# Kernel tuning notes

Hardware: AMD Instinct MI355X
Metric: run time of the kernel (lower is better)

Reference implementation:

```python
import jax, jax.numpy as jnp
import numpy as np

N_NODES = 100000
N_EDGES = 1600000
N_GRAPHS = 5000
F_IN = 11
HID = 128
N_CLASSES = 19


def setup_inputs() -> dict:
    key = jax.random.key(0)
    ks = jax.random.split(key, 12)
    x = jax.random.normal(ks[0], (N_NODES, F_IN), dtype=jnp.float32)
    edge_index = jax.random.randint(ks[1], (2, N_EDGES), 0, N_NODES, dtype=jnp.int64)
    batch = jnp.sort(jax.random.randint(ks[2], (N_NODES,), 0, N_GRAPHS, dtype=jnp.int64))
    def glorot(k, shape):
        lim = float(np.sqrt(6.0 / (shape[0] + shape[1])))
        return jax.random.uniform(k, shape, jnp.float32, -lim, lim)
    return {
        'x': x,
        'edge_index': edge_index,
        'batch': batch,
        'W1': glorot(ks[3], (F_IN, HID)),  'b1': jnp.zeros((HID,), jnp.float32),
        'W2': glorot(ks[4], (HID, HID)),   'b2': jnp.zeros((HID,), jnp.float32),
        'W3': glorot(ks[5], (HID, HID)),   'b3': jnp.zeros((HID,), jnp.float32),
        'Wlin': glorot(ks[6], (HID, N_CLASSES)), 'blin': jnp.zeros((N_CLASSES,), jnp.float32),
    }


def _gcn_conv(x, src, dst, norm, self_w, W, b):
    # GCNConv: D^{-1/2}(A+I)D^{-1/2} X W + b  (self loops handled analytically)
    h = x @ W                                   # [N, out]
    msg = h[src] * norm[:, None]                # [E, out] gathered + scaled
    agg = jax.ops.segment_sum(msg, dst, num_segments=N_NODES)
    return agg + h * self_w[:, None] + b


def reference(x, edge_index, batch, W1, b1, W2, b2, W3, b3, Wlin, blin):
    src, dst = edge_index[0], edge_index[1]
    # degree including self loop (gcn_norm with add_self_loops=True)
    deg = jax.ops.segment_sum(jnp.ones((N_EDGES,), x.dtype), dst, num_segments=N_NODES) + 1.0
    dis = jax.lax.rsqrt(deg)                    # deg^{-1/2}
    norm = dis[src] * dis[dst]                  # per-edge coefficient
    self_w = dis * dis                          # 1/deg for the self loop

    h = jax.nn.relu(_gcn_conv(x, src, dst, norm, self_w, W1, b1))
    h = jax.nn.relu(_gcn_conv(h, src, dst, norm, self_w, W2, b2))
    h = _gcn_conv(h, src, dst, norm, self_w, W3, b3)

    # global_mean_pool over graph ids
    sums = jax.ops.segment_sum(h, batch, num_segments=N_GRAPHS)
    cnts = jax.ops.segment_sum(jnp.ones((N_NODES,), h.dtype), batch, num_segments=N_GRAPHS)
    pooled = sums / jnp.maximum(cnts, 1.0)[:, None]

    # dropout is identity in eval mode
    return pooled @ Wlin + blin
```

## Files before the change

kernel.cpp:

```cpp
#include <hip/hip_runtime.h>
#include <hip/hip_bf16.h>
#include <hip/hip_fp16.h>

#define NN 100000
#define NE 1600000
#define NG 5000
#define FIN 11
#define HID 128
#define NC 19

#define NBK 98
#define BKSH 10
#define BKMASK 1023
#define BCAP 20480
#define CCAP 24576

typedef _Float16 f16x8 __attribute__((ext_vector_type(8)));
typedef float f32x4 __attribute__((ext_vector_type(4)));


__global__ __launch_bounds__(1024) void k_p1scatter(const int* __restrict__ ei,
                                                    int* __restrict__ gcur, unsigned int* __restrict__ p1) {
    __shared__ int hist[NBK];
    __shared__ int base[NBK];
    __shared__ int lrank[NBK];
    int t = threadIdx.x;
    if (t < NBK) { hist[t] = 0; lrank[t] = 0; }
    __syncthreads();

    int e0 = blockIdx.x * 4096 + t * 4;
    int sr[4], dr[4], bk[4];
    if (e0 + 3 < NE) {
        int4 s4 = *(const int4*)(ei + e0);
        int4 d4 = *(const int4*)(ei + NE + e0);
        sr[0] = s4.x; sr[1] = s4.y; sr[2] = s4.z; sr[3] = s4.w;
        dr[0] = d4.x; dr[1] = d4.y; dr[2] = d4.z; dr[3] = d4.w;
        #pragma unroll
        for (int k = 0; k < 4; ++k) { bk[k] = dr[k] >> BKSH; atomicAdd(&hist[bk[k]], 1); }
    } else {
        #pragma unroll
        for (int k = 0; k < 4; ++k) {
            int e = e0 + k;
            if (e < NE) { sr[k] = ei[e]; dr[k] = ei[NE + e]; bk[k] = dr[k] >> BKSH; atomicAdd(&hist[bk[k]], 1); }
            else bk[k] = -1;
        }
    }
    __syncthreads();
    if (t < NBK && hist[t] > 0)
        base[t] = t * BCAP + atomicAdd(&gcur[t], hist[t]);
    __syncthreads();
    #pragma unroll
    for (int k = 0; k < 4; ++k) {
        if (bk[k] >= 0) {
            int slot = atomicAdd(&lrank[bk[k]], 1);
            p1[base[bk[k]] + slot] = (unsigned int)sr[k] | ((unsigned int)(dr[k] & BKMASK) << 17);
        }
    }
}

__global__ __launch_bounds__(1024) void k_p2fill(const unsigned int* __restrict__ p1,
                                                 const int* __restrict__ gcur,
                                                 unsigned int* __restrict__ meta, int* __restrict__ csr,
                                                 float* __restrict__ dis) {
    __shared__ int cnt[1024];
    __shared__ int pf[1024];
    __shared__ int cur[1024];
    __shared__ int wsum[16];
    int bkt = blockIdx.x;
    int t = threadIdx.x;
    int v0 = bkt << BKSH;
    int nb = NN - v0; if (nb > 1024) nb = 1024;
    cnt[t] = 0; cur[t] = 0;
    __syncthreads();
    int count = gcur[bkt]; if (count > BCAP) count = BCAP;
    const unsigned int* reg = p1 + (size_t)bkt * BCAP;
    for (int i = t; i < count; i += 1024)
        atomicAdd(&cnt[reg[i] >> 17], 1);
    __syncthreads();
    int c = cnt[t];
    int pc = (c + 3) & ~3;
    int lane = t & 63, w = t >> 6;
    int val = pc;
    #pragma unroll
    for (int off = 1; off < 64; off <<= 1) {
        int n = __shfl_up(val, off, 64);
        if (lane >= off) val += n;
    }
    if (lane == 63) wsum[w] = val;
    __syncthreads();
    if (w == 0) {
        int s = (lane < 16) ? wsum[lane] : 0;
        #pragma unroll
        for (int off = 1; off < 16; off <<= 1) {
            int n = __shfl_up(s, off, 64);
            if (lane >= off) s += n;
        }
        if (lane < 16) wsum[lane] = s;
    }
    __syncthreads();
    int wbase = (w == 0) ? 0 : wsum[w - 1];
    int excl = wbase + val - pc;
    pf[t] = excl;
    unsigned int gb = (unsigned int)bkt * CCAP;
    if (t < nb) {
        meta[v0 + t] = ((gb + (unsigned int)excl) << 9) | (unsigned int)(pc >> 2);
        dis[v0 + t] = rsqrtf((float)c + 1.0f);
    }
    __syncthreads();
    for (int i = t; i < count; i += 1024) {
        unsigned int u = reg[i];
        int dl = u >> 17;
        int off2 = atomicAdd(&cur[dl], 1);
        csr[gb + pf[dl] + off2] = (int)(u & 0x1FFFFu);
    }
    if (t < nb) {
        int b0 = gb + pf[t];
        for (int k = c; k < pc; ++k) csr[b0 + k] = NN;
    }
}


__global__ __launch_bounds__(256) void k_setup(const float* __restrict__ x, const float* __restrict__ dis,
                                               const int* __restrict__ batch,
                                               const float* __restrict__ W2, const float* __restrict__ W3,
                                               const float* __restrict__ b3, const float* __restrict__ Wl,
                                               const float* __restrict__ bl,
                                               _Float16* __restrict__ xsc, int* __restrict__ gstart,
                                               _Float16* __restrict__ Wp2, float* __restrict__ Wf,
                                               float* __restrict__ bf,
                                               _Float16* __restrict__ Ht, _Float16* __restrict__ tb16) {
    int b = blockIdx.x, t = threadIdx.x;
    if (b < 6251) {
        int i = b * 256 + t;
        if (i < (NN + 1) * 16) {
            int v = i >> 4, c = i & 15;
            float val = (v < NN && c < FIN) ? x[v * FIN + c] * dis[v] : 0.f;
            xsc[i] = (_Float16)val;
        }
    } else if (b < 6271) {
        int g = (b - 6251) * 256 + t;
        if (g > NG) return;
        int lo = 0, hi = NN;
        while (lo < hi) {
            int mid = (lo + hi) >> 1;
            if (batch[mid] < g) lo = mid + 1; else hi = mid;
        }
        gstart[g] = lo;
    } else if (b < 6279) {
        int t2 = (b - 6271) * 256 + t;
        int lane = t2 & 63;
        int tile = t2 >> 6;
        int kb = tile >> 3, ct = tile & 7;
        int kbase = kb * 32 + (lane >> 4) * 8;
        int col = ct * 16 + (lane & 15);
        f16x8 v;
        #pragma unroll
        for (int e = 0; e < 8; ++e) v[e] = (_Float16)W2[(kbase + e) * HID + col];
        *(f16x8*)&Wp2[(size_t)t2 * 8] = v;
    } else if (b < 6312) {
        int i = (b - 6279) * 4 + (t >> 6);
        int tc = t & 63;
        if (tc >= NC || i > HID) return;
        if (i < HID) {
            float a = 0.f;
            #pragma unroll 4
            for (int k = 0; k < HID; ++k) a += W3[i * HID + k] * Wl[k * NC + tc];
            Wf[i * NC + tc] = a;
        } else {
            float a = bl[tc];
            #pragma unroll 4
            for (int k = 0; k < HID; ++k) a += b3[k] * Wl[k * NC + tc];
            bf[tc] = a;
        }
    } else {
        if (t < HID) Ht[(size_t)NN * HID + t] = (_Float16)0.f;
        else tb16[(size_t)NN * HID + (t - HID)] = (_Float16)0.f;
    }
}

__global__ __launch_bounds__(256) void k_l1(const _Float16* __restrict__ xsc,
                                            const unsigned int* __restrict__ meta,
                                            const int* __restrict__ csr, const float* __restrict__ dis,
                                            const float* __restrict__ W1, const float* __restrict__ b1,
                                            _Float16* __restrict__ out16) {
    __shared__ float Ws[FIN][HID];
    __shared__ float Xs[16][17];
    int t = threadIdx.x;
    int row0 = blockIdx.x * 16;
    for (int idx = t; idx < FIN * HID; idx += 256) Ws[idx / HID][idx % HID] = W1[idx];

    int wave = t >> 6, lane = t & 63;
    int erel = lane >> 4, c = lane & 15;
    #pragma unroll
    for (int i = 0; i < 4; ++i) {
        int v = row0 + wave * 4 + i;
        unsigned int m = meta[v];
        int beg = (int)(m >> 9);
        int pend = beg + (int)((m & 511u) << 2);
        float accA = 0.f, accB = 0.f;
        int e = beg;
        for (; e + 8 <= pend; e += 8) {
            int s0 = csr[e + erel], s1 = csr[e + 4 + erel];
            accA += (float)xsc[s0 * 16 + c];
            accB += (float)xsc[s1 * 16 + c];
        }
        if (e < pend) accA += (float)xsc[csr[e + erel] * 16 + c];
        float a = accA + accB;
        a += __shfl_xor(a, 16);
        a += __shfl_xor(a, 32);
        if (erel == 0) {
            a += (float)xsc[v * 16 + c];
            Xs[wave * 4 + i][c] = a * dis[v];
        }
    }
    __syncthreads();
    int cc = t & (HID - 1);
    int rg = t >> 7;
    #pragma unroll
    for (int i = 0; i < 8; ++i) {
        int r = rg * 8 + i;
        int row = row0 + r;
        float a = b1[cc];
        #pragma unroll
        for (int k = 0; k < FIN; ++k) a += Xs[r][k] * Ws[k][cc];
        a = fmaxf(a, 0.f);
        out16[(size_t)row * HID + cc] = (_Float16)(a * dis[row]);
    }
}

__global__ __launch_bounds__(256) void k_agg16(const _Float16* __restrict__ Ht,
                                               const unsigned int* __restrict__ meta,
                                               const int* __restrict__ csr, const float* __restrict__ dis,
                                               _Float16* __restrict__ out16) {
    int wid = threadIdx.x >> 6;
    int lane = threadIdx.x & 63;
    int v = blockIdx.x * 4 + wid;
    if (v >= NN) return;
    int erel = lane >> 4;
    int c8 = lane & 15;
    const _Float16* bp = Ht + (size_t)c8 * 8;
    unsigned int m = meta[v];
    int beg = (int)(m >> 9);
    int pend = beg + (int)((m & 511u) << 2);
    float acc0[8] = {}, acc1[8] = {};
    int e = beg;
    for (; e + 16 <= pend; e += 16) {
        int s0 = csr[e + erel];
        int s1 = csr[e + 4 + erel];
        int s2 = csr[e + 8 + erel];
        int s3 = csr[e + 12 + erel];
        f16x8 h0 = *(const f16x8*)(bp + (size_t)s0 * HID);
        f16x8 h1 = *(const f16x8*)(bp + (size_t)s1 * HID);
        f16x8 h2 = *(const f16x8*)(bp + (size_t)s2 * HID);
        f16x8 h3 = *(const f16x8*)(bp + (size_t)s3 * HID);
        #pragma unroll
        for (int j = 0; j < 8; ++j) {
            acc0[j] += (float)h0[j] + (float)h2[j];
            acc1[j] += (float)h1[j] + (float)h3[j];
        }
    }
    for (; e < pend; e += 4) {
        int s = csr[e + erel];
        f16x8 h = *(const f16x8*)(bp + (size_t)s * HID);
        #pragma unroll
        for (int j = 0; j < 8; ++j) acc0[j] += (float)h[j];
    }
    #pragma unroll
    for (int j = 0; j < 8; ++j) {
        float s = acc0[j] + acc1[j];
        s += __shfl_xor(s, 16);
        s += __shfl_xor(s, 32);
        acc0[j] = s;
    }
    if (erel == 0) {
        f16x8 sh = *(const f16x8*)(bp + (size_t)v * HID);
        float dv = dis[v];
        f16x8 o;
        #pragma unroll
        for (int j = 0; j < 8; ++j) o[j] = (_Float16)((acc0[j] + (float)sh[j]) * dv);
        *(f16x8*)(out16 + (size_t)v * HID + c8 * 8) = o;
    }
}

__global__ __launch_bounds__(256) void k_gemm128m(const _Float16* __restrict__ X,
                                                  const _Float16* __restrict__ Wp,
                                                  const float* __restrict__ bias,
                                                  const float* __restrict__ dis,
                                                  _Float16* __restrict__ out) {
    int wave = threadIdx.x >> 6, lane = threadIdx.x & 63;
    int row0 = blockIdx.x * 128 + wave * 32;
    int rA = lane & 15, kg = lane >> 4;

    f32x4 acc[2][8];
    #pragma unroll
    for (int s = 0; s < 2; ++s)
        #pragma unroll
        for (int c = 0; c < 8; ++c)
            acc[s][c] = {0.f, 0.f, 0.f, 0.f};

    int r0c = row0 + rA;      if (r0c > NN - 1) r0c = NN - 1;
    int r1c = row0 + 16 + rA; if (r1c > NN - 1) r1c = NN - 1;
    const _Float16* xp0 = X + (size_t)r0c * HID + kg * 8;
    const _Float16* xp1 = X + (size_t)r1c * HID + kg * 8;

    #pragma unroll
    for (int kb = 0; kb < 4; ++kb) {
        f16x8 a0 = *(const f16x8*)(xp0 + kb * 32);
        f16x8 a1 = *(const f16x8*)(xp1 + kb * 32);
        #pragma unroll
        for (int ct = 0; ct < 8; ++ct) {
            f16x8 b = *(const f16x8*)&Wp[(size_t)((kb * 8 + ct) * 64 + lane) * 8];
            acc[0][ct] = __builtin_amdgcn_mfma_f32_16x16x32_f16(a0, b, acc[0][ct], 0, 0, 0);
            acc[1][ct] = __builtin_amdgcn_mfma_f32_16x16x32_f16(a1, b, acc[1][ct], 0, 0, 0);
        }
    }

    int c15 = lane & 15;
    #pragma unroll
    for (int s = 0; s < 2; ++s) {
        int rbase = row0 + s * 16 + kg * 4;
        float dv[4];
        #pragma unroll
        for (int r = 0; r < 4; ++r) {
            int rr = rbase + r; if (rr > NN - 1) rr = NN - 1;
            dv[r] = dis[rr];
        }
        #pragma unroll
        for (int ct = 0; ct < 8; ++ct) {
            int col = ct * 16 + c15;
            float bb = bias[col];
            #pragma unroll
            for (int r = 0; r < 4; ++r) {
                int rr = rbase + r;
                if (rr < NN) {
                    float v = fmaxf(acc[s][ct][r] + bb, 0.f) * dv[r];
                    out[(size_t)rr * HID + col] = (_Float16)v;
                }
            }
        }
    }
}

__global__ __launch_bounds__(64) void k_poollin(const _Float16* __restrict__ H, const int* __restrict__ gstart,
                                                const float* __restrict__ Wf, const float* __restrict__ bf,
                                                float* __restrict__ out) {
    int g = blockIdx.x;
    int t = threadIdx.x;
    int beg = gstart[g], end = gstart[g + 1];
    float ax = 0.f, ay = 0.f;
    for (int n = beg; n < end; ++n) {
        ax += (float)H[(size_t)n * HID + t];
        ay += (float)H[(size_t)n * HID + 64 + t];
    }
    float inv = 1.f / fmaxf((float)(end - beg), 1.f);
    __shared__ float ps[HID];
    ps[t] = ax * inv;
    ps[t + 64] = ay * inv;
    __syncthreads();
    if (t < NC) {
        float a = bf[t];
        #pragma unroll 4
        for (int k = 0; k < HID; ++k) a += ps[k] * Wf[k * NC + t];
        out[g * NC + t] = a;
    }
}


extern "C" void kernel_launch(void* const* d_in, const int* in_sizes, int n_in,
                              void* d_out, int out_size, void* d_ws, size_t ws_size,
                              hipStream_t stream) {
    const float* x   = (const float*)d_in[0];
    const int* ei    = (const int*)d_in[1];
    const int* batch = (const int*)d_in[2];
    const float* W1 = (const float*)d_in[3];
    const float* b1 = (const float*)d_in[4];
    const float* W2 = (const float*)d_in[5];
    const float* b2 = (const float*)d_in[6];
    const float* W3 = (const float*)d_in[7];
    const float* b3 = (const float*)d_in[8];
    const float* Wl = (const float*)d_in[9];
    const float* bl = (const float*)d_in[10];
    float* out = (float*)d_out;

    char* ws = (char*)d_ws;
    size_t off = 0;
    auto alloc = [&](size_t bytes) -> void* {
        void* p = ws + off;
        off += (bytes + 255) & ~(size_t)255;
        return p;
    };
    float*        dis    = (float*)alloc((size_t)NN * 4);
    unsigned int* meta   = (unsigned int*)alloc((size_t)NN * 4);
    int*          csr    = (int*)alloc((size_t)NBK * CCAP * 4);
    unsigned int* p1     = (unsigned int*)alloc((size_t)NBK * BCAP * 4);
    int*          gcur   = (int*)alloc(NBK * 4);
    int*          gstart = (int*)alloc((size_t)(NG + 1) * 4);
    _Float16*     xsc    = (_Float16*)alloc((size_t)(NN + 1) * 16 * 2);
    _Float16*     Wp2    = (_Float16*)alloc((size_t)HID * HID * 2);
    float*        Wf     = (float*)alloc((size_t)HID * NC * 4);
    float*        bf     = (float*)alloc(NC * 4);
    _Float16*     Ht     = (_Float16*)alloc((size_t)(NN + 1) * HID * 2);
    _Float16*     tb16   = (_Float16*)alloc((size_t)(NN + 1) * HID * 2);
    (void)ws_size; (void)in_sizes; (void)n_in; (void)out_size;

    hipMemsetAsync(gcur, 0, NBK * 4, stream);

    k_p1scatter<<<(NE + 4095) / 4096, 1024, 0, stream>>>(ei, gcur, p1);
    k_p2fill<<<NBK, 1024, 0, stream>>>(p1, gcur, meta, csr, dis);

    k_setup<<<6313, 256, 0, stream>>>(x, dis, batch, W2, W3, b3, Wl, bl,
                                      xsc, gstart, Wp2, Wf, bf, Ht, tb16);

    k_l1<<<NN / 16, 256, 0, stream>>>(xsc, meta, csr, dis, W1, b1, Ht);

    k_agg16<<<(NN + 3) / 4, 256, 0, stream>>>(Ht, meta, csr, dis, tb16);
    k_gemm128m<<<(NN + 127) / 128, 256, 0, stream>>>(tb16, Wp2, b2, dis, Ht);

    k_agg16<<<(NN + 3) / 4, 256, 0, stream>>>(Ht, meta, csr, dis, tb16);

    k_poollin<<<NG, 64, 0, stream>>>(tb16, gstart, Wf, bf, out);
}
```

Measured before the change: 265.9 us.

## Fuse final aggregation with mean-pool and linear head; halve CSR bucket size

```diff
diff --git a/kernel.cpp b/kernel.cpp
--- a/kernel.cpp
+++ b/kernel.cpp
@@ -9,11 +9,11 @@
 #define HID 128
 #define NC 19
 
-#define NBK 98
-#define BKSH 10
-#define BKMASK 1023
-#define BCAP 20480
-#define CCAP 24576
+#define NBK 196
+#define BKSH 9
+#define BKMASK 511
+#define BCAP 10240
+#define CCAP 12288
 
 typedef _Float16 f16x8 __attribute__((ext_vector_type(8)));
 typedef float f32x4 __attribute__((ext_vector_type(4)));
@@ -62,49 +62,54 @@
                                                  const int* __restrict__ gcur,
                                                  unsigned int* __restrict__ meta, int* __restrict__ csr,
                                                  float* __restrict__ dis) {
-    __shared__ int cnt[1024];
-    __shared__ int pf[1024];
-    __shared__ int cur[1024];
-    __shared__ int wsum[16];
+    __shared__ int cnt[512];
+    __shared__ int pf[512];
+    __shared__ int cur[512];
+    __shared__ int wsum[8];
     int bkt = blockIdx.x;
     int t = threadIdx.x;
     int v0 = bkt << BKSH;
-    int nb = NN - v0; if (nb > 1024) nb = 1024;
-    cnt[t] = 0; cur[t] = 0;
+    int nb = NN - v0; if (nb > 512) nb = 512;
+    unsigned int gb = (unsigned int)bkt * CCAP;
+    if (t < 512) { cnt[t] = 0; cur[t] = 0; }
     __syncthreads();
     int count = gcur[bkt]; if (count > BCAP) count = BCAP;
     const unsigned int* reg = p1 + (size_t)bkt * BCAP;
     for (int i = t; i < count; i += 1024)
         atomicAdd(&cnt[reg[i] >> 17], 1);
     __syncthreads();
-    int c = cnt[t];
-    int pc = (c + 3) & ~3;
+    int c = 0, pc = 0, val = 0;
     int lane = t & 63, w = t >> 6;
-    int val = pc;
-    #pragma unroll
-    for (int off = 1; off < 64; off <<= 1) {
-        int n = __shfl_up(val, off, 64);
-        if (lane >= off) val += n;
-    }
-    if (lane == 63) wsum[w] = val;
+    if (t < 512) {
+        c = cnt[t];
+        pc = (c + 3) & ~3;
+        val = pc;
+        #pragma unroll
+        for (int off = 1; off < 64; off <<= 1) {
+            int n = __shfl_up(val, off, 64);
+            if (lane >= off) val += n;
+        }
+        if (lane == 63) wsum[w] = val;
+    }
     __syncthreads();
     if (w == 0) {
-        int s = (lane < 16) ? wsum[lane] : 0;
-        #pragma unroll
-        for (int off = 1; off < 16; off <<= 1) {
+        int s = (lane < 8) ? wsum[lane] : 0;
+        #pragma unroll
+        for (int off = 1; off < 8; off <<= 1) {
             int n = __shfl_up(s, off, 64);
             if (lane >= off) s += n;
         }
-        if (lane < 16) wsum[lane] = s;
-    }
-    __syncthreads();
-    int wbase = (w == 0) ? 0 : wsum[w - 1];
-    int excl = wbase + val - pc;
-    pf[t] = excl;
-    unsigned int gb = (unsigned int)bkt * CCAP;
-    if (t < nb) {
-        meta[v0 + t] = ((gb + (unsigned int)excl) << 9) | (unsigned int)(pc >> 2);
-        dis[v0 + t] = rsqrtf((float)c + 1.0f);
+        if (lane < 8) wsum[lane] = s;
+    }
+    __syncthreads();
+    if (t < 512) {
+        int wbase = (w == 0) ? 0 : wsum[w - 1];
+        int excl = wbase + val - pc;
+        pf[t] = excl;
+        if (t < nb) {
+            meta[v0 + t] = ((gb + (unsigned int)excl) << 9) | (unsigned int)(pc >> 2);
+            dis[v0 + t] = rsqrtf((float)c + 1.0f);
+        }
     }
     __syncthreads();
     for (int i = t; i < count; i += 1024) {
@@ -128,7 +133,7 @@
                                                _Float16* __restrict__ xsc, int* __restrict__ gstart,
                                                _Float16* __restrict__ Wp2, float* __restrict__ Wf,
                                                float* __restrict__ bf,
-                                               _Float16* __restrict__ Ht, _Float16* __restrict__ tb16) {
+                                               _Float16* __restrict__ Ht) {
     int b = blockIdx.x, t = threadIdx.x;
     if (b < 6251) {
         int i = b * 256 + t;
@@ -174,9 +179,9 @@
         }
     } else {
         if (t < HID) Ht[(size_t)NN * HID + t] = (_Float16)0.f;
-        else tb16[(size_t)NN * HID + (t - HID)] = (_Float16)0.f;
-    }
-}
+    }
+}
+
 
 __global__ __launch_bounds__(256) void k_l1(const _Float16* __restrict__ xsc,
                                             const unsigned int* __restrict__ meta,
@@ -227,6 +232,7 @@
         out16[(size_t)row * HID + cc] = (_Float16)(a * dis[row]);
     }
 }
+
 
 __global__ __launch_bounds__(256) void k_agg16(const _Float16* __restrict__ Ht,
                                                const unsigned int* __restrict__ meta,
@@ -282,6 +288,7 @@
     }
 }
 
+
 __global__ __launch_bounds__(256) void k_gemm128m(const _Float16* __restrict__ X,
                                                   const _Float16* __restrict__ Wp,
                                                   const float* __restrict__ bias,
@@ -341,27 +348,61 @@
     }
 }
 
-__global__ __launch_bounds__(64) void k_poollin(const _Float16* __restrict__ H, const int* __restrict__ gstart,
-                                                const float* __restrict__ Wf, const float* __restrict__ bf,
-                                                float* __restrict__ out) {
-    int g = blockIdx.x;
-    int t = threadIdx.x;
-    int beg = gstart[g], end = gstart[g + 1];
-    float ax = 0.f, ay = 0.f;
-    for (int n = beg; n < end; ++n) {
-        ax += (float)H[(size_t)n * HID + t];
-        ay += (float)H[(size_t)n * HID + 64 + t];
-    }
-    float inv = 1.f / fmaxf((float)(end - beg), 1.f);
-    __shared__ float ps[HID];
-    ps[t] = ax * inv;
-    ps[t + 64] = ay * inv;
-    __syncthreads();
-    if (t < NC) {
-        float a = bf[t];
+__global__ __launch_bounds__(256) void k_aggpool(const _Float16* __restrict__ Ht,
+                                                 const unsigned int* __restrict__ meta,
+                                                 const int* __restrict__ csr, const float* __restrict__ dis,
+                                                 const int* __restrict__ gstart,
+                                                 const float* __restrict__ Wf, const float* __restrict__ bf,
+                                                 float* __restrict__ out) {
+    __shared__ float ps[4][HID];
+    int wid = threadIdx.x >> 6, lane = threadIdx.x & 63;
+    int g = blockIdx.x * 4 + wid;
+    int erel = lane >> 4, c8 = lane & 15;
+    const _Float16* bp = Ht + (size_t)c8 * 8;
+    int nbeg = gstart[g], nend = gstart[g + 1];
+    float gacc[8] = {};
+    for (int v = nbeg; v < nend; ++v) {
+        unsigned int m = meta[v];
+        int beg = (int)(m >> 9);
+        int pend = beg + (int)((m & 511u) << 2);
+        float dv = dis[v];
+        float va[8] = {}, vb[8] = {};
+        for (int e = beg; e < pend; e += 8) {
+            int i1 = e + erel;
+            int i2 = e + 4 + erel;
+            int s1 = csr[i1];
+            int s2 = (i2 < pend) ? csr[i2] : NN;
+            f16x8 h1 = *(const f16x8*)(bp + (size_t)s1 * HID);
+            f16x8 h2 = *(const f16x8*)(bp + (size_t)s2 * HID);
+            #pragma unroll
+            for (int j = 0; j < 8; ++j) { va[j] += (float)h1[j]; vb[j] += (float)h2[j]; }
+        }
+        if (erel == 0) {
+            f16x8 hv = *(const f16x8*)(bp + (size_t)v * HID);
+            #pragma unroll
+            for (int j = 0; j < 8; ++j) va[j] += (float)hv[j];
+        }
+        #pragma unroll
+        for (int j = 0; j < 8; ++j) gacc[j] += dv * (va[j] + vb[j]);
+    }
+    #pragma unroll
+    for (int j = 0; j < 8; ++j) {
+        float s = gacc[j];
+        s += __shfl_xor(s, 16);
+        s += __shfl_xor(s, 32);
+        gacc[j] = s;
+    }
+    float inv = 1.f / fmaxf((float)(nend - nbeg), 1.f);
+    if (erel == 0) {
+        #pragma unroll
+        for (int j = 0; j < 8; ++j) ps[wid][c8 * 8 + j] = gacc[j] * inv;
+    }
+    __syncthreads();
+    if (lane < NC) {
+        float a = bf[lane];
         #pragma unroll 4
-        for (int k = 0; k < HID; ++k) a += ps[k] * Wf[k * NC + t];
-        out[g * NC + t] = a;
+        for (int k = 0; k < HID; ++k) a += ps[wid][k] * Wf[k * NC + lane];
+        out[g * NC + lane] = a;
     }
 }
 
@@ -409,14 +450,12 @@
     k_p2fill<<<NBK, 1024, 0, stream>>>(p1, gcur, meta, csr, dis);
 
     k_setup<<<6313, 256, 0, stream>>>(x, dis, batch, W2, W3, b3, Wl, bl,
-                                      xsc, gstart, Wp2, Wf, bf, Ht, tb16);
+                                      xsc, gstart, Wp2, Wf, bf, Ht);
 
     k_l1<<<NN / 16, 256, 0, stream>>>(xsc, meta, csr, dis, W1, b1, Ht);
 
     k_agg16<<<(NN + 3) / 4, 256, 0, stream>>>(Ht, meta, csr, dis, tb16);
     k_gemm128m<<<(NN + 127) / 128, 256, 0, stream>>>(tb16, Wp2, b2, dis, Ht);
 
-    k_agg16<<<(NN + 3) / 4, 256, 0, stream>>>(Ht, meta, csr, dis, tb16);
-
-    k_poollin<<<NG, 64, 0, stream>>>(tb16, gstart, Wf, bf, out);
-}
+    k_aggpool<<<NG / 4, 256, 0, stream>>>(Ht, meta, csr, dis, gstart, Wf, bf, out);
+}
```

Result: slower. 282.0 us (+6.0%).
